# Kernel tuning notes

Measured on AMD Instinct MI355X. Metric: run time of the kernel, lower is better.

Reference implementation:

```python
import jax, jax.numpy as jnp
import numpy as np

D = 768      # qkv.in_features (ViT-Base)
R = 16       # LoRA rank
T = 8        # task_id: number of previously saved adapters
B_, S_ = 32, 256
TAU = 1.0


def setup_inputs() -> dict:
    key = jax.random.key(0)
    ks = jax.random.split(key, 13)
    s = lambda k, shape, sc=0.02: jax.random.normal(k, shape, jnp.float32) * sc
    return {
        "x": jax.random.normal(ks[0], (B_, S_, D), jnp.float32),
        "qkv_w": s(ks[1], (3 * D, D)),           # torch Linear weight [out,in]
        "qkv_b": s(ks[2], (3 * D,)),
        "la_q": s(ks[3], (R, D)),                # current-task LoRA A_q [r,d]
        "lb_q": s(ks[4], (D, R)),                # current-task LoRA B_q [d,r]
        "la_v": s(ks[5], (R, D)),
        "lb_v": s(ks[6], (D, R)),
        "A_q": s(ks[7], (T, R, D)),              # saved per-task A_q stacks
        "B_q": s(ks[8], (T, D, R)),
        "A_v": s(ks[9], (T, R, D)),
        "B_v": s(ks[10], (T, D, R)),
        "gate_logits": jax.random.normal(ks[11], (T,), jnp.float32),
        "alpha": jnp.ones((T + 1,), jnp.float32),  # gumbel_gate.alpha, indexed by task_id
    }


def _moe_branch(x, A, B, beta):
    """Weighted sum over T tasks of (x @ A_t^T @ B_t^T) / (||A_t||*||B_t||), weight beta_t.

    Vectorizes the per-task serial low-rank matmuls of the torch loop into two
    batched einsums; beta/norm scaling is folded into B to avoid materializing
    per-task [B,S,D] outputs.
    """
    nA = jnp.sqrt(jnp.sum(A * A, axis=(1, 2)))   # [T] Frobenius norms
    nB = jnp.sqrt(jnp.sum(B * B, axis=(1, 2)))
    scale = beta / (nA * nB)                      # [T]
    za = jnp.einsum('bsd,trd->bstr', x, A)       # [B,S,T,r]
    Bs = B * scale[:, None, None]                 # [T,D,r]
    return jnp.einsum('bstr,tdr->bsd', za, Bs)   # [B,S,D]


def _lora(x, a, b):
    # torch: b(a(x)) with Linear weights a:[r,d], b:[d,r]
    return jnp.einsum('bsr,dr->bsd', jnp.einsum('bsd,rd->bsr', x, a), b)


def reference(x, qkv_w, qkv_b, la_q, lb_q, la_v, lb_v, A_q, B_q, A_v, B_v, gate_logits, alpha):
    # Gumbel-softmax gate over tasks (deterministic/eval path: softmax(logits/tau), hard=False)
    beta = jax.nn.softmax(gate_logits / TAU)
    a_cur = alpha[T]  # alpha[self.task_id]
    new_q = _moe_branch(x, A_q, B_q, beta) + a_cur * _lora(x, la_q, lb_q)
    new_v = _moe_branch(x, A_v, B_v, beta) + a_cur * _lora(x, la_v, lb_v)
    qkv = jnp.einsum('bsd,ed->bse', x, qkv_w) + qkv_b  # [B,S,3D]
    qkv = qkv.at[..., :D].add(new_q)
    qkv = qkv.at[..., 2 * D:].add(new_v)
    return qkv
```

## Files before the change

kernel.cpp:

```cpp
#include <hip/hip_runtime.h>

#define TOK 8192
#define DD  768
#define NOUT 2304
#define TT  8
#define RR  16
#define KRANK 144

typedef __bf16 bf16;
typedef __bf16 bf16x4 __attribute__((ext_vector_type(4)));
typedef __bf16 bf16x8 __attribute__((ext_vector_type(8)));
typedef float  floatx4 __attribute__((ext_vector_type(4)));

__device__ __forceinline__ void gl_lds16(const void* g, void* l) {
    __builtin_amdgcn_global_load_lds((const __attribute__((address_space(1))) void*)g,
                                     (__attribute__((address_space(3))) void*)l, 16, 0, 0);
}

__global__ __launch_bounds__(256) void prep_kernel(
    const float* __restrict__ A_q, const float* __restrict__ B_q,
    const float* __restrict__ A_v, const float* __restrict__ B_v,
    const float* __restrict__ x, bf16* __restrict__ xb,
    float* __restrict__ norms)
{
    __shared__ float ws4[4];
    const int b = blockIdx.x;
    if (b < 32) {
        const float* base;
        switch (b >> 3) {
            case 0: base = A_q; break;
            case 1: base = B_q; break;
            case 2: base = A_v; break;
            default: base = B_v; break;
        }
        base += (b & 7) * (RR * DD);
        float s = 0.f;
        for (int i = threadIdx.x; i < RR * DD; i += 256) {
            float v = base[i];
            s = fmaf(v, v, s);
        }
        #pragma unroll
        for (int off = 32; off > 0; off >>= 1) s += __shfl_down(s, off);
        if ((threadIdx.x & 63) == 0) ws4[threadIdx.x >> 6] = s;
        __syncthreads();
        if (threadIdx.x == 0)
            norms[b] = sqrtf(ws4[0] + ws4[1] + ws4[2] + ws4[3]);
    } else {
        const int idx = ((b - 32) * 256 + threadIdx.x) * 4;
        const float4 v = *(const float4*)(x + idx);
        bf16x4 o = { (bf16)v.x, (bf16)v.y, (bf16)v.z, (bf16)v.w };
        *(bf16x4*)(xb + idx) = o;
    }
}

__global__ __launch_bounds__(256) void fold_kernel(
    const float* __restrict__ qkv_w,
    const float* __restrict__ A_q, const float* __restrict__ la_q,
    const float* __restrict__ B_q, const float* __restrict__ lb_q,
    const float* __restrict__ A_v, const float* __restrict__ la_v,
    const float* __restrict__ B_v, const float* __restrict__ lb_v,
    const float* __restrict__ gate_logits, const float* __restrict__ alpha,
    const float* __restrict__ norms, bf16* __restrict__ Wc)
{
    const int tid = threadIdx.x;
    const int d = blockIdx.x * 256 + tid;
    const int gy = blockIdx.y;

    if (gy >= 96 && gy < 192) {
        const int rowbase = DD + (gy - 96) * 8;
        #pragma unroll
        for (int j = 0; j < 8; ++j) {
            const int row = rowbase + j;
            Wc[row * DD + d] = (bf16)qkv_w[row * DD + d];
        }
        return;
    }

    __shared__ float c_lds[8 * KRANK];
    __shared__ float sc_sh[TT];
    __shared__ float acur_sh;

    const bool is_v = (gy >= 192);
    const int e0 = (is_v ? gy - 192 : gy) * 8;
    const float* Astack = is_v ? A_v : A_q;
    const float* la     = is_v ? la_v : la_q;
    const float* Bmat   = is_v ? B_v : B_q;
    const float* lb     = is_v ? lb_v : lb_q;
    const float* nA     = norms + (is_v ? 16 : 0);
    const float* nB     = norms + (is_v ? 24 : 8);
    const int rowbase   = (is_v ? 2 * DD : 0) + e0;

    if (tid == 0) {
        float mx = gate_logits[0];
        for (int t = 1; t < TT; ++t) mx = fmaxf(mx, gate_logits[t]);
        float e[TT], s = 0.f;
        for (int t = 0; t < TT; ++t) { e[t] = __expf(gate_logits[t] - mx); s += e[t]; }
        for (int t = 0; t < TT; ++t) sc_sh[t] = (e[t] / s) / (nA[t] * nB[t]);
        acur_sh = alpha[TT];
    }
    __syncthreads();

    for (int idx = tid; idx < 8 * KRANK; idx += 256) {
        const int j = idx / KRANK, i = idx - j * KRANK;
        const int e = e0 + j;
        float v;
        if (i < TT * RR) {
            const int t = i >> 4, r = i & 15;
            v = sc_sh[t] * Bmat[(t * DD + e) * RR + r];
        } else {
            v = acur_sh * lb[e * RR + (i - TT * RR)];
        }
        c_lds[j * KRANK + i] = v;
    }
    __syncthreads();

    float acc[8] = {0.f, 0.f, 0.f, 0.f, 0.f, 0.f, 0.f, 0.f};

    for (int i = 0; i < TT * RR; i += 4) {
        const float a0 = Astack[(i + 0) * DD + d];
        const float a1 = Astack[(i + 1) * DD + d];
        const float a2 = Astack[(i + 2) * DD + d];
        const float a3 = Astack[(i + 3) * DD + d];
        #pragma unroll
        for (int j = 0; j < 8; ++j) {
            const float4 cv = *(const float4*)&c_lds[j * KRANK + i];
            acc[j] = fmaf(a0, cv.x, fmaf(a1, cv.y, fmaf(a2, cv.z, fmaf(a3, cv.w, acc[j]))));
        }
    }
    #pragma unroll
    for (int i = 0; i < RR; i += 4) {
        const float a0 = la[(i + 0) * DD + d];
        const float a1 = la[(i + 1) * DD + d];
        const float a2 = la[(i + 2) * DD + d];
        const float a3 = la[(i + 3) * DD + d];
        #pragma unroll
        for (int j = 0; j < 8; ++j) {
            const float4 cv = *(const float4*)&c_lds[j * KRANK + TT * RR + i];
            acc[j] = fmaf(a0, cv.x, fmaf(a1, cv.y, fmaf(a2, cv.z, fmaf(a3, cv.w, acc[j]))));
        }
    }

    #pragma unroll
    for (int j = 0; j < 8; ++j) {
        const int row = rowbase + j;
        Wc[row * DD + d] = (bf16)(qkv_w[row * DD + d] + acc[j]);
    }
}

__global__ __launch_bounds__(256, 2) void gemm_kernel(
    const bf16* __restrict__ A, const bf16* __restrict__ B,
    const float* __restrict__ bias, float* __restrict__ C)
{
    __shared__ __align__(16) char smem[53248];
    bf16* lds_a = (bf16*)smem;
    bf16* lds_b = (bf16*)(smem + 16384);

    const int tid  = threadIdx.x;
    const int lane = tid & 63;
    const int wave = tid >> 6;

    const int flat  = blockIdx.x;
    const int xcd   = flat & 7;
    const int local = flat >> 3;
    const int mb    = xcd * 8 + (local & 7);
    const int nb    = local >> 3;
    const int m0 = mb * 128;
    const int n0 = nb * 288;

    const int wm = (wave >> 1) * 64;
    const int wn = (wave & 1) * 144;

    const int srow = lane >> 3;
    const int scol = ((lane & 7) ^ srow) * 8;

    floatx4 acc[4][9];
    #pragma unroll
    for (int i = 0; i < 4; ++i)
        #pragma unroll
        for (int j = 0; j < 9; ++j)
            acc[i][j] = (floatx4){0.f, 0.f, 0.f, 0.f};

    for (int kt = 0; kt < DD / 64; ++kt) {
        const int k0 = kt * 64;
        #pragma unroll
        for (int i = 0; i < 4; ++i) {
            const int j = i * 4 + wave;
            gl_lds16(A + (m0 + j * 8 + srow) * DD + k0 + scol, &lds_a[j * 512]);
        }
        #pragma unroll
        for (int i = 0; i < 9; ++i) {
            const int j = i * 4 + wave;
            gl_lds16(B + (n0 + j * 8 + srow) * DD + k0 + scol, &lds_b[j * 512]);
        }
        __syncthreads();

        #pragma unroll
        for (int ks = 0; ks < 2; ++ks) {
            const int c_log = ks * 4 + (lane >> 4);
            bf16x8 af[4];
            #pragma unroll
            for (int mt = 0; mt < 4; ++mt) {
                const int r = wm + mt * 16 + (lane & 15);
                af[mt] = *(const bf16x8*)&lds_a[r * 64 + ((c_log ^ (r & 7)) * 8)];
            }
            #pragma unroll
            for (int nt = 0; nt < 9; ++nt) {
                const int r = wn + nt * 16 + (lane & 15);
                const bf16x8 bfr = *(const bf16x8*)&lds_b[r * 64 + ((c_log ^ (r & 7)) * 8)];
                #pragma unroll
                for (int mt = 0; mt < 4; ++mt)
                    acc[mt][nt] = __builtin_amdgcn_mfma_f32_16x16x32_bf16(
                        af[mt], bfr, acc[mt][nt], 0, 0, 0);
            }
        }
        __syncthreads();
    }

    const int cr = (lane >> 4) * 4;
    const int cc = lane & 15;
    #pragma unroll
    for (int nt = 0; nt < 9; ++nt) {
        const int gn = n0 + wn + nt * 16 + cc;
        const float bv = bias[gn];
        #pragma unroll
        for (int mt = 0; mt < 4; ++mt) {
            const int gmb = m0 + wm + mt * 16 + cr;
            #pragma unroll
            for (int r = 0; r < 4; ++r)
                C[(gmb + r) * NOUT + gn] = acc[mt][nt][r] + bv;
        }
    }
}

extern "C" void kernel_launch(void* const* d_in, const int* in_sizes, int n_in,
                              void* d_out, int out_size, void* d_ws, size_t ws_size,
                              hipStream_t stream)
{
    const float* x           = (const float*)d_in[0];
    const float* qkv_w       = (const float*)d_in[1];
    const float* qkv_b       = (const float*)d_in[2];
    const float* la_q        = (const float*)d_in[3];
    const float* lb_q        = (const float*)d_in[4];
    const float* la_v        = (const float*)d_in[5];
    const float* lb_v        = (const float*)d_in[6];
    const float* A_q         = (const float*)d_in[7];
    const float* B_q         = (const float*)d_in[8];
    const float* A_v         = (const float*)d_in[9];
    const float* B_v         = (const float*)d_in[10];
    const float* gate_logits = (const float*)d_in[11];
    const float* alpha       = (const float*)d_in[12];
    float* out = (float*)d_out;

    char* ws = (char*)d_ws;
    bf16*  Xbf    = (bf16*)ws;
    bf16*  Wc     = (bf16*)(ws + 12582912);
    float* norms  = (float*)(ws + 12582912 + 3538944);

    prep_kernel<<<32 + TOK * DD / 1024, 256, 0, stream>>>(A_q, B_q, A_v, B_v,
                                                          x, Xbf, norms);
    fold_kernel<<<dim3(3, 288), 256, 0, stream>>>(qkv_w,
                                                  A_q, la_q, B_q, lb_q,
                                                  A_v, la_v, B_v, lb_v,
                                                  gate_logits, alpha, norms, Wc);
    gemm_kernel<<<512, 256, 0, stream>>>(Xbf, Wc, qkv_b, out);
}
```

Baseline: 171.6 us.

## Double-buffer GEMM LDS tiles, shrink N tile to 144, widen prep conversion

The GEMM now stages the next K-tile into a second LDS buffer using async global-to-LDS loads while it computes on the current one, with manual vmcnt waits and barriers in place of __syncthreads. The N tile drops from 288 to 144 and each wave owns a 32-row slab, which doubles the grid to 1024 blocks and halves accumulator registers. The prep kernel converts 8 floats per thread instead of 4. The larger LDS footprint (68KB) may limit how many blocks fit per CU, and the smaller tile reloads each A tile more often.

Result: slower. 176.8 us (+3.0%).

```diff
diff --git a/kernel.cpp b/kernel.cpp
--- a/kernel.cpp
+++ b/kernel.cpp
@@ -46,10 +46,12 @@
         if (threadIdx.x == 0)
             norms[b] = sqrtf(ws4[0] + ws4[1] + ws4[2] + ws4[3]);
     } else {
-        const int idx = ((b - 32) * 256 + threadIdx.x) * 4;
-        const float4 v = *(const float4*)(x + idx);
-        bf16x4 o = { (bf16)v.x, (bf16)v.y, (bf16)v.z, (bf16)v.w };
-        *(bf16x4*)(xb + idx) = o;
+        const int idx = ((b - 32) * 256 + threadIdx.x) * 8;
+        const float4 v0 = *(const float4*)(x + idx);
+        const float4 v1 = *(const float4*)(x + idx + 4);
+        bf16x8 o = { (bf16)v0.x, (bf16)v0.y, (bf16)v0.z, (bf16)v0.w,
+                     (bf16)v1.x, (bf16)v1.y, (bf16)v1.z, (bf16)v1.w };
+        *(bf16x8*)(xb + idx) = o;
     }
 }
 
@@ -151,9 +153,9 @@
     const bf16* __restrict__ A, const bf16* __restrict__ B,
     const float* __restrict__ bias, float* __restrict__ C)
 {
-    __shared__ __align__(16) char smem[53248];
-    bf16* lds_a = (bf16*)smem;
-    bf16* lds_b = (bf16*)(smem + 16384);
+    __shared__ __align__(16) char smem[69632];
+    bf16* const lds_a = (bf16*)smem;
+    bf16* const lds_b = (bf16*)(smem + 32768);
 
     const int tid  = threadIdx.x;
     const int lane = tid & 63;
@@ -165,69 +167,82 @@
     const int mb    = xcd * 8 + (local & 7);
     const int nb    = local >> 3;
     const int m0 = mb * 128;
-    const int n0 = nb * 288;
-
-    const int wm = (wave >> 1) * 64;
-    const int wn = (wave & 1) * 144;
+    const int n0 = nb * 144;
+
+    const int wm = wave * 32;
 
     const int srow = lane >> 3;
     const int scol = ((lane & 7) ^ srow) * 8;
 
-    floatx4 acc[4][9];
-    #pragma unroll
-    for (int i = 0; i < 4; ++i)
+    floatx4 acc[2][9];
+    #pragma unroll
+    for (int i = 0; i < 2; ++i)
         #pragma unroll
         for (int j = 0; j < 9; ++j)
             acc[i][j] = (floatx4){0.f, 0.f, 0.f, 0.f};
 
-    for (int kt = 0; kt < DD / 64; ++kt) {
-        const int k0 = kt * 64;
-        #pragma unroll
-        for (int i = 0; i < 4; ++i) {
-            const int j = i * 4 + wave;
-            gl_lds16(A + (m0 + j * 8 + srow) * DD + k0 + scol, &lds_a[j * 512]);
-        }
-        #pragma unroll
-        for (int i = 0; i < 9; ++i) {
-            const int j = i * 4 + wave;
-            gl_lds16(B + (n0 + j * 8 + srow) * DD + k0 + scol, &lds_b[j * 512]);
-        }
-        __syncthreads();
-
+    const bf16* const gA = A + (m0 + srow) * DD + scol;
+    const bf16* const gB = B + (n0 + srow) * DD + scol;
+
+    auto stage = [&](int buf, int k0) {
+        bf16* la = lds_a + buf * (128 * 64);
+        bf16* lb = lds_b + buf * (144 * 64);
+        for (int c = wave; c < 34; c += 4) {
+            if (c < 16) gl_lds16(gA + c * 8 * DD + k0, la + c * 512);
+            else        gl_lds16(gB + (c - 16) * 8 * DD + k0, lb + (c - 16) * 512);
+        }
+    };
+
+    stage(0, 0);
+
+    for (int kt = 0; kt < 12; ++kt) {
+        const int cur = kt & 1;
+        if (kt < 11) {
+            stage(cur ^ 1, (kt + 1) * 64);
+            asm volatile("s_waitcnt vmcnt(8)" ::: "memory");
+        } else {
+            asm volatile("s_waitcnt vmcnt(0)" ::: "memory");
+        }
+        __builtin_amdgcn_s_barrier();
+        asm volatile("" ::: "memory");
+
+        const bf16* la = lds_a + cur * (128 * 64);
+        const bf16* lb = lds_b + cur * (144 * 64);
         #pragma unroll
         for (int ks = 0; ks < 2; ++ks) {
             const int c_log = ks * 4 + (lane >> 4);
-            bf16x8 af[4];
+            bf16x8 af[2];
             #pragma unroll
-            for (int mt = 0; mt < 4; ++mt) {
+            for (int mt = 0; mt < 2; ++mt) {
                 const int r = wm + mt * 16 + (lane & 15);
-                af[mt] = *(const bf16x8*)&lds_a[r * 64 + ((c_log ^ (r & 7)) * 8)];
+                af[mt] = *(const bf16x8*)&la[r * 64 + ((c_log ^ (r & 7)) * 8)];
             }
             #pragma unroll
             for (int nt = 0; nt < 9; ++nt) {
-                const int r = wn + nt * 16 + (lane & 15);
-                const bf16x8 bfr = *(const bf16x8*)&lds_b[r * 64 + ((c_log ^ (r & 7)) * 8)];
+                const int r = nt * 16 + (lane & 15);
+                const bf16x8 bfr = *(const bf16x8*)&lb[r * 64 + ((c_log ^ (r & 7)) * 8)];
                 #pragma unroll
-                for (int mt = 0; mt < 4; ++mt)
+                for (int mt = 0; mt < 2; ++mt)
                     acc[mt][nt] = __builtin_amdgcn_mfma_f32_16x16x32_bf16(
                         af[mt], bfr, acc[mt][nt], 0, 0, 0);
             }
         }
-        __syncthreads();
+        asm volatile("" ::: "memory");
+        __builtin_amdgcn_s_barrier();
     }
 
     const int cr = (lane >> 4) * 4;
     const int cc = lane & 15;
     #pragma unroll
     for (int nt = 0; nt < 9; ++nt) {
-        const int gn = n0 + wn + nt * 16 + cc;
+        const int gn = n0 + nt * 16 + cc;
         const float bv = bias[gn];
         #pragma unroll
-        for (int mt = 0; mt < 4; ++mt) {
-            const int gmb = m0 + wm + mt * 16 + cr;
+        for (int mt = 0; mt < 2; ++mt) {
+            const int gm = m0 + wm + mt * 16 + cr;
             #pragma unroll
             for (int r = 0; r < 4; ++r)
-                C[(gmb + r) * NOUT + gn] = acc[mt][nt][r] + bv;
+                C[(gm + r) * NOUT + gn] = acc[mt][nt][r] + bv;
         }
     }
 }
@@ -256,11 +271,11 @@
     bf16*  Wc     = (bf16*)(ws + 12582912);
     float* norms  = (float*)(ws + 12582912 + 3538944);
 
-    prep_kernel<<<32 + TOK * DD / 1024, 256, 0, stream>>>(A_q, B_q, A_v, B_v,
+    prep_kernel<<<32 + TOK * DD / 2048, 256, 0, stream>>>(A_q, B_q, A_v, B_v,
                                                           x, Xbf, norms);
     fold_kernel<<<dim3(3, 288), 256, 0, stream>>>(qkv_w,
                                                   A_q, la_q, B_q, lb_q,
                                                   A_v, la_v, B_v, lb_v,
                                                   gate_logits, alpha, norms, Wc);
-    gemm_kernel<<<512, 256, 0, stream>>>(Xbf, Wc, qkv_b, out);
-}
+    gemm_kernel<<<1024, 256, 0, stream>>>(Xbf, Wc, qkv_b, out);
+}
```

## Double-buffer GEMM LDS staging with BK=32 and widen x conversion to 8 elements

Applied to the files above, without the earlier changes.

The GEMM main loop moves from a single-buffered 64-wide K tile with two full syncthreads per step to a double-buffered 32-wide K tile. The next tile is prefetched via global_load_lds while MFMAs run on the current one, using explicit vmcnt waits and raw s_barrier. The LDS layout and swizzle are changed to match the 32-wide rows. The prep kernel now converts 8 floats per thread instead of 4, halving its grid. The cost is more loop iterations and barriers, plus the hand-coded vmcnt(6) count must match how many loads each wave issues.

Measured after the change: 176.8 us. +3.0%, slower.

```diff
diff --git a/kernel.cpp b/kernel.cpp
--- a/kernel.cpp
+++ b/kernel.cpp
@@ -46,10 +46,12 @@
         if (threadIdx.x == 0)
             norms[b] = sqrtf(ws4[0] + ws4[1] + ws4[2] + ws4[3]);
     } else {
-        const int idx = ((b - 32) * 256 + threadIdx.x) * 4;
-        const float4 v = *(const float4*)(x + idx);
-        bf16x4 o = { (bf16)v.x, (bf16)v.y, (bf16)v.z, (bf16)v.w };
-        *(bf16x4*)(xb + idx) = o;
+        const int idx = ((b - 32) * 256 + threadIdx.x) * 8;
+        const float4 v0 = *(const float4*)(x + idx);
+        const float4 v1 = *(const float4*)(x + idx + 4);
+        bf16x8 o = { (bf16)v0.x, (bf16)v0.y, (bf16)v0.z, (bf16)v0.w,
+                     (bf16)v1.x, (bf16)v1.y, (bf16)v1.z, (bf16)v1.w };
+        *(bf16x8*)(xb + idx) = o;
     }
 }
 
@@ -152,8 +154,8 @@
     const float* __restrict__ bias, float* __restrict__ C)
 {
     __shared__ __align__(16) char smem[53248];
-    bf16* lds_a = (bf16*)smem;
-    bf16* lds_b = (bf16*)(smem + 16384);
+    bf16* const lds_a = (bf16*)smem;
+    bf16* const lds_b = (bf16*)(smem + 16384);
 
     const int tid  = threadIdx.x;
     const int lane = tid & 63;
@@ -170,8 +172,8 @@
     const int wm = (wave >> 1) * 64;
     const int wn = (wave & 1) * 144;
 
-    const int srow = lane >> 3;
-    const int scol = ((lane & 7) ^ srow) * 8;
+    const int srow = lane >> 2;
+    const int scol = ((lane & 3) ^ (srow & 3)) * 8;
 
     floatx4 acc[4][9];
     #pragma unroll
@@ -180,40 +182,52 @@
         for (int j = 0; j < 9; ++j)
             acc[i][j] = (floatx4){0.f, 0.f, 0.f, 0.f};
 
-    for (int kt = 0; kt < DD / 64; ++kt) {
-        const int k0 = kt * 64;
-        #pragma unroll
-        for (int i = 0; i < 4; ++i) {
-            const int j = i * 4 + wave;
-            gl_lds16(A + (m0 + j * 8 + srow) * DD + k0 + scol, &lds_a[j * 512]);
-        }
-        #pragma unroll
-        for (int i = 0; i < 9; ++i) {
-            const int j = i * 4 + wave;
-            gl_lds16(B + (n0 + j * 8 + srow) * DD + k0 + scol, &lds_b[j * 512]);
-        }
-        __syncthreads();
-
-        #pragma unroll
-        for (int ks = 0; ks < 2; ++ks) {
-            const int c_log = ks * 4 + (lane >> 4);
-            bf16x8 af[4];
+    const bf16* const gA = A + (m0 + srow) * DD + scol;
+    const bf16* const gB = B + (n0 + srow) * DD + scol;
+
+    auto stage = [&](int buf, int k0) {
+        bf16* la = lds_a + buf * (128 * 32);
+        bf16* lb = lds_b + buf * (288 * 32);
+        for (int c = wave; c < 26; c += 4) {
+            if (c < 8) gl_lds16(gA + c * 16 * DD + k0, la + c * 512);
+            else       gl_lds16(gB + (c - 8) * 16 * DD + k0, lb + (c - 8) * 512);
+        }
+    };
+
+    stage(0, 0);
+
+    for (int kt = 0; kt < 24; ++kt) {
+        const int cur = kt & 1;
+        if (kt < 23) {
+            stage(cur ^ 1, (kt + 1) * 32);
+            asm volatile("s_waitcnt vmcnt(6)" ::: "memory");
+        } else {
+            asm volatile("s_waitcnt vmcnt(0)" ::: "memory");
+        }
+        __builtin_amdgcn_s_barrier();
+        asm volatile("" ::: "memory");
+
+        const bf16* la = lds_a + cur * (128 * 32);
+        const bf16* lb = lds_b + cur * (288 * 32);
+        const int c_log = lane >> 4;
+        const int swz = (c_log ^ (lane & 3)) * 8;
+        bf16x8 af[4];
+        #pragma unroll
+        for (int mt = 0; mt < 4; ++mt) {
+            const int r = wm + mt * 16 + (lane & 15);
+            af[mt] = *(const bf16x8*)&la[r * 32 + swz];
+        }
+        #pragma unroll
+        for (int nt = 0; nt < 9; ++nt) {
+            const int r = wn + nt * 16 + (lane & 15);
+            const bf16x8 bfr = *(const bf16x8*)&lb[r * 32 + swz];
             #pragma unroll
-            for (int mt = 0; mt < 4; ++mt) {
-                const int r = wm + mt * 16 + (lane & 15);
-                af[mt] = *(const bf16x8*)&lds_a[r * 64 + ((c_log ^ (r & 7)) * 8)];
-            }
-            #pragma unroll
-            for (int nt = 0; nt < 9; ++nt) {
-                const int r = wn + nt * 16 + (lane & 15);
-                const bf16x8 bfr = *(const bf16x8*)&lds_b[r * 64 + ((c_log ^ (r & 7)) * 8)];
-                #pragma unroll
-                for (int mt = 0; mt < 4; ++mt)
-                    acc[mt][nt] = __builtin_amdgcn_mfma_f32_16x16x32_bf16(
-                        af[mt], bfr, acc[mt][nt], 0, 0, 0);
-            }
-        }
-        __syncthreads();
+            for (int mt = 0; mt < 4; ++mt)
+                acc[mt][nt] = __builtin_amdgcn_mfma_f32_16x16x32_bf16(
+                    af[mt], bfr, acc[mt][nt], 0, 0, 0);
+        }
+        asm volatile("" ::: "memory");
+        __builtin_amdgcn_s_barrier();
     }
 
     const int cr = (lane >> 4) * 4;
@@ -256,7 +270,7 @@
     bf16*  Wc     = (bf16*)(ws + 12582912);
     float* norms  = (float*)(ws + 12582912 + 3538944);
 
-    prep_kernel<<<32 + TOK * DD / 1024, 256, 0, stream>>>(A_q, B_q, A_v, B_v,
+    prep_kernel<<<32 + TOK * DD / 2048, 256, 0, stream>>>(A_q, B_q, A_v, B_v,
                                                           x, Xbf, norms);
     fold_kernel<<<dim3(3, 288), 256, 0, stream>>>(qkv_w,
                                                   A_q, la_q, B_q, lb_q,
```
